# Kernel optimization log

Measured on AMD Instinct MI355X. Metric: run time of the kernel, lower is better.

Reference implementation:

```python
import jax, jax.numpy as jnp
import numpy as np

E = 524288
B = 16
NODE_IN = 128
EDGE_IN = 64
GLOBAL_IN = 64
HIDDEN = 256
EDGE_OUT = 64
CAT_IN = EDGE_IN + 2 * NODE_IN + GLOBAL_IN  # 384


def setup_inputs() -> dict:
    key = jax.random.key(0)
    ks = jax.random.split(key, 9)
    src = jax.random.normal(ks[0], (E, NODE_IN), dtype=jnp.float32)
    dest = jax.random.normal(ks[1], (E, NODE_IN), dtype=jnp.float32)
    edge_attr = jax.random.normal(ks[2], (E, EDGE_IN), dtype=jnp.float32)
    u = jax.random.normal(ks[3], (B, GLOBAL_IN), dtype=jnp.float32)
    batch = jnp.sort(jax.random.randint(ks[4], (E,), 0, B, dtype=jnp.int64))
    # MLP params (torch Linear default init scale ~1/sqrt(fan_in))
    W1 = jax.random.normal(ks[5], (CAT_IN, HIDDEN), dtype=jnp.float32) / np.sqrt(CAT_IN)
    b1 = jax.random.normal(ks[6], (HIDDEN,), dtype=jnp.float32) / np.sqrt(CAT_IN)
    W2 = jax.random.normal(ks[7], (HIDDEN, EDGE_OUT), dtype=jnp.float32) / np.sqrt(HIDDEN)
    b2 = jax.random.normal(ks[8], (EDGE_OUT,), dtype=jnp.float32) / np.sqrt(HIDDEN)
    return {"src": src, "dest": dest, "edge_attr": edge_attr, "u": u,
            "batch": batch, "W1": W1, "b1": b1, "W2": W2, "b2": b2}


def reference(src, dest, edge_attr, u, batch, W1, b1, W2, b2):
    # gather global features per edge, concat, 2-layer MLP with ReLU
    x = jnp.concatenate([src, dest, edge_attr, u[batch]], axis=1)  # [E, 384]
    h = jax.nn.relu(x @ W1 + b1)                                   # [E, hidden]
    return h @ W2 + b2                                             # [E, edge_out]
```

## Files before the change

kernel.cpp:

```cpp
#include <hip/hip_runtime.h>

typedef __bf16 bf16_t;
typedef bf16_t bf16x8 __attribute__((ext_vector_type(8)));
typedef bf16_t bf16x4 __attribute__((ext_vector_type(4)));
typedef float f32x4 __attribute__((ext_vector_type(4)));
typedef unsigned short u16;
typedef unsigned int u32;

#define E_TOT 524288
#define MT 64
#define NBLK (E_TOT / MT)

__device__ __forceinline__ u16 f2bf(float f) {
  u32 u = __builtin_bit_cast(u32, f);
  u += 0x7FFFu + ((u >> 16) & 1u);
  return (u16)(u >> 16);
}

__device__ __forceinline__ bf16x8 pack8(f32x4 a, f32x4 b) {
  bf16x8 p;
  p[0] = (bf16_t)a[0]; p[1] = (bf16_t)a[1]; p[2] = (bf16_t)a[2]; p[3] = (bf16_t)a[3];
  p[4] = (bf16_t)b[0]; p[5] = (bf16_t)b[1]; p[6] = (bf16_t)b[2]; p[7] = (bf16_t)b[3];
  return p;
}

__global__ void prep_w1f(const float* __restrict__ W1, u16* __restrict__ W1F) {
  int t = blockIdx.x * 256 + threadIdx.x;
  if (t < 98304) {
    int e  = t & 7;
    int l  = (t >> 3) & 63;
    int nf = (t >> 9) & 3;
    int wc = (t >> 11) & 3;
    int kb = t >> 13;
    int n = wc * 64 + nf * 16 + (l & 15);
    int k = kb * 32 + ((l >> 4) << 3) + e;
    W1F[t] = f2bf(W1[k * 256 + n]);
  }
}

__global__ void prep_w2f(const float* __restrict__ W2, u16* __restrict__ W2F) {
  int t = blockIdx.x * 256 + threadIdx.x;
  if (t < 16384) {
    int e   = t & 7;
    int l   = (t >> 3) & 63;
    int n2f = (t >> 9) & 3;
    int ks  = t >> 11;
    int n2 = n2f * 16 + (l & 15);
    int k  = ks * 32 + ((l >> 4) << 3) + e;
    W2F[t] = f2bf(W2[k * 64 + n2]);
  }
}

__global__ void __launch_bounds__(256) edge_fused(
    const float* __restrict__ src, const float* __restrict__ dst,
    const float* __restrict__ ea, const float* __restrict__ u,
    const int* __restrict__ batch, const u16* __restrict__ W1F,
    const float* __restrict__ b1, const u16* __restrict__ W2F,
    const float* __restrict__ b2, float* __restrict__ out)
{
  __shared__ __align__(16) u16 smem[16384];
  u16* As = smem;
  u16* Hs = smem;

  const int t    = threadIdx.x;
  const int wid  = t >> 6;
  const int lane = t & 63;
  const int lr   = lane & 15;
  const int lg   = lane >> 4;
  const int e0   = blockIdx.x * MT;
  const int r    = t >> 2;
  const int jc   = t & 3;
  const int bidx = batch[e0 + r];
  const int u0   = 2 * jc;

  auto loadA = [&](int c, f32x4* ra) {
    const float* p;
    if (c < 2)       p = src + (size_t)(e0 + r) * 128 + c * 64 + jc * 16;
    else if (c < 4)  p = dst + (size_t)(e0 + r) * 128 + (c - 2) * 64 + jc * 16;
    else if (c == 4) p = ea + (size_t)(e0 + r) * 64 + jc * 16;
    else             p = u + (size_t)bidx * 64 + jc * 16;
    ra[0] = *(const f32x4*)p;
    ra[1] = *(const f32x4*)(p + 4);
    ra[2] = *(const f32x4*)(p + 8);
    ra[3] = *(const f32x4*)(p + 12);
  };
  auto loadW1 = [&](int c, bf16x8* wf) {
    #pragma unroll
    for (int ks = 0; ks < 2; ++ks) {
      const u16* p = W1F + ((size_t)((2 * c + ks) * 4 + wid) * 4) * 512 + lane * 8;
      wf[ks * 4 + 0] = *(const bf16x8*)(p);
      wf[ks * 4 + 1] = *(const bf16x8*)(p + 512);
      wf[ks * 4 + 2] = *(const bf16x8*)(p + 1024);
      wf[ks * 4 + 3] = *(const bf16x8*)(p + 1536);
    }
  };

  f32x4 ra[4];
  bf16x8 wf[8];
  loadA(0, ra);
  loadW1(0, wf);

  f32x4 acc[4][4];
  #pragma unroll
  for (int i = 0; i < 4; ++i)
    #pragma unroll
    for (int j = 0; j < 4; ++j)
      acc[i][j] = (f32x4){0.f, 0.f, 0.f, 0.f};

  #pragma unroll
  for (int kb = 0; kb < 6; ++kb) {
    u16* Ab = As + (kb & 1) * 4096;

    {
      bf16x8 lo = pack8(ra[0], ra[1]);
      bf16x8 hi = pack8(ra[2], ra[3]);
      *(bf16x8*)&Ab[(r * 8 + (u0 ^ (r & 7))) * 8]       = lo;
      *(bf16x8*)&Ab[(r * 8 + ((u0 + 1) ^ (r & 7))) * 8] = hi;
    }
    if (kb < 5) loadA(kb + 1, ra);

    asm volatile("s_waitcnt lgkmcnt(0)" ::: "memory");
    __builtin_amdgcn_s_barrier();
    __builtin_amdgcn_sched_barrier(0);

    __builtin_amdgcn_s_setprio(1);
    #pragma unroll
    for (int ks = 0; ks < 2; ++ks) {
      bf16x8 af[4];
      #pragma unroll
      for (int mf = 0; mf < 4; ++mf) {
        int row = mf * 16 + lr;
        af[mf] = *(const bf16x8*)&Ab[(row * 8 + ((ks * 4 + lg) ^ (row & 7))) * 8];
      }
      #pragma unroll
      for (int nf = 0; nf < 4; ++nf)
        #pragma unroll
        for (int mf = 0; mf < 4; ++mf)
          acc[nf][mf] = __builtin_amdgcn_mfma_f32_16x16x32_bf16(wf[ks * 4 + nf], af[mf], acc[nf][mf], 0, 0, 0);
    }
    __builtin_amdgcn_s_setprio(0);

    if (kb < 5) loadW1(kb + 1, wf);
  }
  __syncthreads();

  #pragma unroll
  for (int nf = 0; nf < 4; ++nf) {
    f32x4 b1v = *(const f32x4*)(b1 + wid * 64 + nf * 16 + lg * 4);
    #pragma unroll
    for (int mf = 0; mf < 4; ++mf) {
      int row = mf * 16 + lr;
      bf16x4 hb;
      #pragma unroll
      for (int rr = 0; rr < 4; ++rr)
        hb[rr] = (bf16_t)fmaxf(acc[nf][mf][rr] + b1v[rr], 0.f);
      int uu = (wid * 4 + nf) * 4 + lg;
      int up = uu ^ ((lr & 3) << 2);
      *(bf16x4*)&Hs[row * 256 + up * 4] = hb;
    }
  }
  __syncthreads();

  const int row2 = wid * 16 + lr;
  f32x4 d2[4];
  #pragma unroll
  for (int i = 0; i < 4; ++i) d2[i] = (f32x4){0.f, 0.f, 0.f, 0.f};
  #pragma unroll
  for (int ks = 0; ks < 8; ++ks) {
    int uu = ks * 8 + lg * 2;
    int up = uu ^ ((lr & 3) << 2);
    bf16x8 a2 = *(const bf16x8*)&Hs[row2 * 256 + up * 4];
    const u16* q = W2F + (size_t)ks * 2048 + lane * 8;
    #pragma unroll
    for (int n2f = 0; n2f < 4; ++n2f)
      d2[n2f] = __builtin_amdgcn_mfma_f32_16x16x32_bf16(
          *(const bf16x8*)(q + n2f * 512), a2, d2[n2f], 0, 0, 0);
  }

  #pragma unroll
  for (int n2f = 0; n2f < 4; ++n2f) {
    f32x4 b2v = *(const f32x4*)(b2 + n2f * 16 + lg * 4);
    f32x4 ov = d2[n2f] + b2v;
    *(f32x4*)&out[(size_t)(e0 + row2) * 64 + n2f * 16 + lg * 4] = ov;
  }
}

extern "C" void kernel_launch(void* const* d_in, const int* in_sizes, int n_in,
                              void* d_out, int out_size, void* d_ws, size_t ws_size,
                              hipStream_t stream) {
  const float* src  = (const float*)d_in[0];
  const float* dst  = (const float*)d_in[1];
  const float* ea   = (const float*)d_in[2];
  const float* u    = (const float*)d_in[3];
  const int* batch  = (const int*)d_in[4];
  const float* W1   = (const float*)d_in[5];
  const float* b1   = (const float*)d_in[6];
  const float* W2   = (const float*)d_in[7];
  const float* b2   = (const float*)d_in[8];
  float* out = (float*)d_out;

  u16* W1F = (u16*)d_ws;
  u16* W2F = W1F + 98304;

  prep_w1f<<<384, 256, 0, stream>>>(W1, W1F);
  prep_w2f<<<64, 256, 0, stream>>>(W2, W2F);
  edge_fused<<<NBLK, 256, 0, stream>>>(src, dst, ea, u, batch, W1F, b1, W2F, b2, out);
}
```

Measured before the change: 243.6 us.

## Make edge kernel persistent over several tiles with cross-tile prefetch

Each block now processes 8 consecutive 64-edge tiles in a loop instead of one, cutting the grid by 8x. Input loads are double-buffered two chunks ahead, and the first chunks and W1 fragments of the next tile are prefetched during the tail of the current tile, so global loads overlap the MFMA and epilogue phases. The cost is more registers for the extra prefetch buffer and far fewer blocks, which may leave CUs underfilled or idle at the tail and lowers occupancy.

```diff
diff --git a/kernel.cpp b/kernel.cpp
--- a/kernel.cpp
+++ b/kernel.cpp
@@ -9,7 +9,8 @@
 
 #define E_TOT 524288
 #define MT 64
-#define NBLK (E_TOT / MT)
+#define TPB 8
+#define NBLK (E_TOT / (MT * TPB))
 
 __device__ __forceinline__ u16 f2bf(float f) {
   u32 u = __builtin_bit_cast(u32, f);
@@ -67,18 +68,18 @@
   const int lane = t & 63;
   const int lr   = lane & 15;
   const int lg   = lane >> 4;
-  const int e0   = blockIdx.x * MT;
   const int r    = t >> 2;
   const int jc   = t & 3;
-  const int bidx = batch[e0 + r];
   const int u0   = 2 * jc;
-
-  auto loadA = [&](int c, f32x4* ra) {
+  const int eb0  = blockIdx.x * (MT * TPB);
+
+  auto loadA = [&](int c, int ebase, f32x4* ra) {
+    size_t er = (size_t)(ebase + r);
     const float* p;
-    if (c < 2)       p = src + (size_t)(e0 + r) * 128 + c * 64 + jc * 16;
-    else if (c < 4)  p = dst + (size_t)(e0 + r) * 128 + (c - 2) * 64 + jc * 16;
-    else if (c == 4) p = ea + (size_t)(e0 + r) * 64 + jc * 16;
-    else             p = u + (size_t)bidx * 64 + jc * 16;
+    if (c < 2)       p = src + er * 128 + c * 64 + jc * 16;
+    else if (c < 4)  p = dst + er * 128 + (c - 2) * 64 + jc * 16;
+    else if (c == 4) p = ea + er * 64 + jc * 16;
+    else             p = u + (size_t)batch[er] * 64 + jc * 16;
     ra[0] = *(const f32x4*)p;
     ra[1] = *(const f32x4*)(p + 4);
     ra[2] = *(const f32x4*)(p + 8);
@@ -95,93 +96,113 @@
     }
   };
 
-  f32x4 ra[4];
+  f32x4 ra[4], rb[4];
   bf16x8 wf[8];
-  loadA(0, ra);
+  loadA(0, eb0, ra);
+  loadA(1, eb0, rb);
   loadW1(0, wf);
 
-  f32x4 acc[4][4];
-  #pragma unroll
-  for (int i = 0; i < 4; ++i)
-    #pragma unroll
-    for (int j = 0; j < 4; ++j)
-      acc[i][j] = (f32x4){0.f, 0.f, 0.f, 0.f};
-
-  #pragma unroll
-  for (int kb = 0; kb < 6; ++kb) {
-    u16* Ab = As + (kb & 1) * 4096;
-
-    {
-      bf16x8 lo = pack8(ra[0], ra[1]);
-      bf16x8 hi = pack8(ra[2], ra[3]);
-      *(bf16x8*)&Ab[(r * 8 + (u0 ^ (r & 7))) * 8]       = lo;
-      *(bf16x8*)&Ab[(r * 8 + ((u0 + 1) ^ (r & 7))) * 8] = hi;
-    }
-    if (kb < 5) loadA(kb + 1, ra);
+  for (int tile = 0; tile < TPB; ++tile) {
+    const int eb = eb0 + tile * MT;
+
+    f32x4 acc[4][4];
+    #pragma unroll
+    for (int i = 0; i < 4; ++i)
+      #pragma unroll
+      for (int j = 0; j < 4; ++j)
+        acc[i][j] = (f32x4){0.f, 0.f, 0.f, 0.f};
+
+    #pragma unroll
+    for (int c = 0; c < 6; ++c) {
+      f32x4* cur = (c & 1) ? rb : ra;
+      u16* Ab = As + (c & 1) * 4096;
+
+      {
+        bf16x8 lo = pack8(cur[0], cur[1]);
+        bf16x8 hi = pack8(cur[2], cur[3]);
+        *(bf16x8*)&Ab[(r * 8 + (u0 ^ (r & 7))) * 8]       = lo;
+        *(bf16x8*)&Ab[(r * 8 + ((u0 + 1) ^ (r & 7))) * 8] = hi;
+      }
+      if (c < 4)            loadA(c + 2, eb, cur);
+      else if (tile < TPB - 1) {
+        if (c == 4) loadA(0, eb + MT, cur);
+        else        loadA(1, eb + MT, cur);
+      }
+
+      asm volatile("s_waitcnt lgkmcnt(0)" ::: "memory");
+      __builtin_amdgcn_s_barrier();
+      __builtin_amdgcn_sched_barrier(0);
+
+      __builtin_amdgcn_s_setprio(1);
+      #pragma unroll
+      for (int ks = 0; ks < 2; ++ks) {
+        bf16x8 af[4];
+        #pragma unroll
+        for (int mf = 0; mf < 4; ++mf) {
+          int row = mf * 16 + lr;
+          af[mf] = *(const bf16x8*)&Ab[(row * 8 + ((ks * 4 + lg) ^ (row & 7))) * 8];
+        }
+        #pragma unroll
+        for (int nf = 0; nf < 4; ++nf)
+          #pragma unroll
+          for (int mf = 0; mf < 4; ++mf)
+            acc[nf][mf] = __builtin_amdgcn_mfma_f32_16x16x32_bf16(wf[ks * 4 + nf], af[mf], acc[nf][mf], 0, 0, 0);
+      }
+      __builtin_amdgcn_s_setprio(0);
+
+      if (c < 5)                loadW1(c + 1, wf);
+      else if (tile < TPB - 1)  loadW1(0, wf);
+    }
 
     asm volatile("s_waitcnt lgkmcnt(0)" ::: "memory");
     __builtin_amdgcn_s_barrier();
     __builtin_amdgcn_sched_barrier(0);
 
-    __builtin_amdgcn_s_setprio(1);
-    #pragma unroll
-    for (int ks = 0; ks < 2; ++ks) {
-      bf16x8 af[4];
+    #pragma unroll
+    for (int nf = 0; nf < 4; ++nf) {
+      f32x4 b1v = *(const f32x4*)(b1 + wid * 64 + nf * 16 + lg * 4);
       #pragma unroll
       for (int mf = 0; mf < 4; ++mf) {
+        bf16x4 hb;
+        #pragma unroll
+        for (int rr = 0; rr < 4; ++rr)
+          hb[rr] = (bf16_t)fmaxf(acc[nf][mf][rr] + b1v[rr], 0.f);
         int row = mf * 16 + lr;
-        af[mf] = *(const bf16x8*)&Ab[(row * 8 + ((ks * 4 + lg) ^ (row & 7))) * 8];
-      }
-      #pragma unroll
-      for (int nf = 0; nf < 4; ++nf)
-        #pragma unroll
-        for (int mf = 0; mf < 4; ++mf)
-          acc[nf][mf] = __builtin_amdgcn_mfma_f32_16x16x32_bf16(wf[ks * 4 + nf], af[mf], acc[nf][mf], 0, 0, 0);
-    }
-    __builtin_amdgcn_s_setprio(0);
-
-    if (kb < 5) loadW1(kb + 1, wf);
-  }
-  __syncthreads();
-
-  #pragma unroll
-  for (int nf = 0; nf < 4; ++nf) {
-    f32x4 b1v = *(const f32x4*)(b1 + wid * 64 + nf * 16 + lg * 4);
-    #pragma unroll
-    for (int mf = 0; mf < 4; ++mf) {
-      int row = mf * 16 + lr;
-      bf16x4 hb;
-      #pragma unroll
-      for (int rr = 0; rr < 4; ++rr)
-        hb[rr] = (bf16_t)fmaxf(acc[nf][mf][rr] + b1v[rr], 0.f);
-      int uu = (wid * 4 + nf) * 4 + lg;
+        int uu = (wid * 4 + nf) * 4 + lg;
+        int up = uu ^ ((lr & 3) << 2);
+        *(bf16x4*)&Hs[row * 256 + up * 4] = hb;
+      }
+    }
+    asm volatile("s_waitcnt lgkmcnt(0)" ::: "memory");
+    __builtin_amdgcn_s_barrier();
+    __builtin_amdgcn_sched_barrier(0);
+
+    const int row2 = wid * 16 + lr;
+    f32x4 d2[4];
+    #pragma unroll
+    for (int i = 0; i < 4; ++i) d2[i] = (f32x4){0.f, 0.f, 0.f, 0.f};
+    #pragma unroll
+    for (int ks = 0; ks < 8; ++ks) {
+      int uu = ks * 8 + lg * 2;
       int up = uu ^ ((lr & 3) << 2);
-      *(bf16x4*)&Hs[row * 256 + up * 4] = hb;
-    }
-  }
-  __syncthreads();
-
-  const int row2 = wid * 16 + lr;
-  f32x4 d2[4];
-  #pragma unroll
-  for (int i = 0; i < 4; ++i) d2[i] = (f32x4){0.f, 0.f, 0.f, 0.f};
-  #pragma unroll
-  for (int ks = 0; ks < 8; ++ks) {
-    int uu = ks * 8 + lg * 2;
-    int up = uu ^ ((lr & 3) << 2);
-    bf16x8 a2 = *(const bf16x8*)&Hs[row2 * 256 + up * 4];
-    const u16* q = W2F + (size_t)ks * 2048 + lane * 8;
-    #pragma unroll
-    for (int n2f = 0; n2f < 4; ++n2f)
-      d2[n2f] = __builtin_amdgcn_mfma_f32_16x16x32_bf16(
-          *(const bf16x8*)(q + n2f * 512), a2, d2[n2f], 0, 0, 0);
-  }
-
-  #pragma unroll
-  for (int n2f = 0; n2f < 4; ++n2f) {
-    f32x4 b2v = *(const f32x4*)(b2 + n2f * 16 + lg * 4);
-    f32x4 ov = d2[n2f] + b2v;
-    *(f32x4*)&out[(size_t)(e0 + row2) * 64 + n2f * 16 + lg * 4] = ov;
+      bf16x8 a2 = *(const bf16x8*)&Hs[row2 * 256 + up * 4];
+      const u16* q = W2F + (size_t)ks * 2048 + lane * 8;
+      #pragma unroll
+      for (int n2f = 0; n2f < 4; ++n2f)
+        d2[n2f] = __builtin_amdgcn_mfma_f32_16x16x32_bf16(
+            *(const bf16x8*)(q + n2f * 512), a2, d2[n2f], 0, 0, 0);
+    }
+
+    #pragma unroll
+    for (int n2f = 0; n2f < 4; ++n2f) {
+      f32x4 b2v = *(const f32x4*)(b2 + n2f * 16 + lg * 4);
+      f32x4 ov = d2[n2f] + b2v;
+      *(f32x4*)&out[(size_t)(eb + row2) * 64 + n2f * 16 + lg * 4] = ov;
+    }
+
+    asm volatile("s_waitcnt lgkmcnt(0)" ::: "memory");
+    __builtin_amdgcn_s_barrier();
+    __builtin_amdgcn_sched_barrier(0);
   }
 }
 
```

After: 405.9 us. +66.6%, slower.

## Enlarge edge tile to 128 rows with 8 waves and LDS-staged W1 pipeline

Applied to the files above, without the earlier changes.

Doubles the block tile to 128 edges with 512 threads in a 2x4 wave grid. W1 is now staged into LDS with global_load_lds, double-buffered and swizzled, rather than each wave loading its fragments from global memory into registers. A three-deep register prefetch of A chunks is added, the N dimension is split into two halves separated by barriers, and block indices are remapped so consecutive blocks are spread across the edge range. The aim is better W1 reuse across more rows and more overlap of loads with MFMA, at the cost of 96KB of LDS per block, which lowers occupancy, plus more barriers.

```diff
diff --git a/kernel.cpp b/kernel.cpp
--- a/kernel.cpp
+++ b/kernel.cpp
@@ -8,8 +8,8 @@
 typedef unsigned int u32;
 
 #define E_TOT 524288
-#define MT 64
-#define NBLK (E_TOT / MT)
+#define BM 128
+#define NBLK (E_TOT / BM)
 
 __device__ __forceinline__ u16 f2bf(float f) {
   u32 u = __builtin_bit_cast(u32, f);
@@ -24,17 +24,22 @@
   return p;
 }
 
-__global__ void prep_w1f(const float* __restrict__ W1, u16* __restrict__ W1F) {
+__device__ __forceinline__ void gload_lds16(const void* g, void* l) {
+  __builtin_amdgcn_global_load_lds(
+      (const __attribute__((address_space(1))) u32*)g,
+      (__attribute__((address_space(3))) u32*)l, 16, 0, 0);
+}
+
+__global__ void prep_w1c(const float* __restrict__ W1, u16* __restrict__ W1c) {
   int t = blockIdx.x * 256 + threadIdx.x;
   if (t < 98304) {
-    int e  = t & 7;
-    int l  = (t >> 3) & 63;
-    int nf = (t >> 9) & 3;
-    int wc = (t >> 11) & 3;
-    int kb = t >> 13;
-    int n = wc * 64 + nf * 16 + (l & 15);
-    int k = kb * 32 + ((l >> 4) << 3) + e;
-    W1F[t] = f2bf(W1[k * 256 + n]);
+    int e = t & 7;
+    int U = t >> 3;
+    int kb = U >> 11, rem = U & 2047;
+    int n = rem >> 3, jswz = rem & 7;
+    int j = jswz ^ (n & 7);
+    int k = kb * 64 + j * 8 + e;
+    W1c[t] = f2bf(W1[k * 256 + n]);
   }
 }
 
@@ -51,15 +56,14 @@
   }
 }
 
-__global__ void __launch_bounds__(256) edge_fused(
+__global__ void __launch_bounds__(512) edge_fused(
     const float* __restrict__ src, const float* __restrict__ dst,
     const float* __restrict__ ea, const float* __restrict__ u,
-    const int* __restrict__ batch, const u16* __restrict__ W1F,
+    const int* __restrict__ batch, const u16* __restrict__ W1c,
     const float* __restrict__ b1, const u16* __restrict__ W2F,
     const float* __restrict__ b2, float* __restrict__ out)
 {
-  __shared__ __align__(16) u16 smem[16384];
-  u16* As = smem;
+  __shared__ __align__(16) u16 smem[49152];
   u16* Hs = smem;
 
   const int t    = threadIdx.x;
@@ -67,38 +71,51 @@
   const int lane = t & 63;
   const int lr   = lane & 15;
   const int lg   = lane >> 4;
-  const int e0   = blockIdx.x * MT;
+  const int wr   = wid >> 2;
+  const int wc   = wid & 3;
+  const int bid  = blockIdx.x;
+  const int e0   = ((bid & 7) * 512 + (bid >> 3)) * BM;
   const int r    = t >> 2;
   const int jc   = t & 3;
+  const int j0   = 2 * jc;
   const int bidx = batch[e0 + r];
-  const int u0   = 2 * jc;
-
-  auto loadA = [&](int c, f32x4* ra) {
+
+  auto loadA = [&](int c, f32x4* s) {
     const float* p;
     if (c < 2)       p = src + (size_t)(e0 + r) * 128 + c * 64 + jc * 16;
     else if (c < 4)  p = dst + (size_t)(e0 + r) * 128 + (c - 2) * 64 + jc * 16;
     else if (c == 4) p = ea + (size_t)(e0 + r) * 64 + jc * 16;
     else             p = u + (size_t)bidx * 64 + jc * 16;
-    ra[0] = *(const f32x4*)p;
-    ra[1] = *(const f32x4*)(p + 4);
-    ra[2] = *(const f32x4*)(p + 8);
-    ra[3] = *(const f32x4*)(p + 12);
+    s[0] = *(const f32x4*)p;
+    s[1] = *(const f32x4*)(p + 4);
+    s[2] = *(const f32x4*)(p + 8);
+    s[3] = *(const f32x4*)(p + 12);
   };
-  auto loadW1 = [&](int c, bf16x8* wf) {
-    #pragma unroll
-    for (int ks = 0; ks < 2; ++ks) {
-      const u16* p = W1F + ((size_t)((2 * c + ks) * 4 + wid) * 4) * 512 + lane * 8;
-      wf[ks * 4 + 0] = *(const bf16x8*)(p);
-      wf[ks * 4 + 1] = *(const bf16x8*)(p + 512);
-      wf[ks * 4 + 2] = *(const bf16x8*)(p + 1024);
-      wf[ks * 4 + 3] = *(const bf16x8*)(p + 1536);
+  auto issueW = [&](int c, u16* Wn) {
+    #pragma unroll
+    for (int g = 0; g < 4; ++g) {
+      int ub = wid * 256 + g * 64;
+      gload_lds16(W1c + ((size_t)c * 2048 + ub + lane) * 8, Wn + ub * 8);
     }
   };
-
-  f32x4 ra[4];
-  bf16x8 wf[8];
-  loadA(0, ra);
-  loadW1(0, wf);
+  auto packWrite = [&](f32x4* s, u16* An) {
+    bf16x8 lo = pack8(s[0], s[1]);
+    bf16x8 hi = pack8(s[2], s[3]);
+    *(bf16x8*)&An[(r * 8 + (j0 ^ (r & 7))) * 8]       = lo;
+    *(bf16x8*)&An[(r * 8 + ((j0 + 1) ^ (r & 7))) * 8] = hi;
+  };
+
+  f32x4 aset[3][4];
+  loadA(0, aset[0]);
+  loadA(1, aset[1]);
+  issueW(0, smem + 16384);
+  loadA(2, aset[2]);
+  asm volatile("s_waitcnt vmcnt(12)" ::: "memory");
+  packWrite(aset[0], smem);
+  asm volatile("s_waitcnt vmcnt(4)" ::: "memory");
+  asm volatile("s_waitcnt lgkmcnt(0)" ::: "memory");
+  __builtin_amdgcn_sched_barrier(0);
+  __builtin_amdgcn_s_barrier();
 
   f32x4 acc[4][4];
   #pragma unroll
@@ -109,57 +126,89 @@
 
   #pragma unroll
   for (int kb = 0; kb < 6; ++kb) {
-    u16* Ab = As + (kb & 1) * 4096;
-
-    {
-      bf16x8 lo = pack8(ra[0], ra[1]);
-      bf16x8 hi = pack8(ra[2], ra[3]);
-      *(bf16x8*)&Ab[(r * 8 + (u0 ^ (r & 7))) * 8]       = lo;
-      *(bf16x8*)&Ab[(r * 8 + ((u0 + 1) ^ (r & 7))) * 8] = hi;
-    }
-    if (kb < 5) loadA(kb + 1, ra);
+    u16* Ab = smem + ((kb & 1) << 13);
+    u16* An = smem + (((kb + 1) & 1) << 13);
+    u16* Wb = smem + 16384 + ((kb & 1) << 14);
+    u16* Wn = smem + 16384 + (((kb + 1) & 1) << 14);
+
+    bf16x8 af[2][4];
+    #pragma unroll
+    for (int ks = 0; ks < 2; ++ks)
+      #pragma unroll
+      for (int mf = 0; mf < 4; ++mf) {
+        int row = wr * 64 + mf * 16 + lr;
+        af[ks][mf] = *(const bf16x8*)&Ab[(row * 8 + ((ks * 4 + lg) ^ (row & 7))) * 8];
+      }
+    bf16x8 wf0[2][2];
+    #pragma unroll
+    for (int ks = 0; ks < 2; ++ks)
+      #pragma unroll
+      for (int nfi = 0; nfi < 2; ++nfi) {
+        int n = wc * 64 + nfi * 16 + lr;
+        wf0[ks][nfi] = *(const bf16x8*)&Wb[(n * 8 + ((ks * 4 + lg) ^ (n & 7))) * 8];
+      }
+    if (kb < 5) issueW(kb + 1, Wn);
 
     asm volatile("s_waitcnt lgkmcnt(0)" ::: "memory");
-    __builtin_amdgcn_s_barrier();
     __builtin_amdgcn_sched_barrier(0);
-
+    __builtin_amdgcn_s_barrier();
     __builtin_amdgcn_s_setprio(1);
     #pragma unroll
-    for (int ks = 0; ks < 2; ++ks) {
-      bf16x8 af[4];
-      #pragma unroll
-      for (int mf = 0; mf < 4; ++mf) {
-        int row = mf * 16 + lr;
-        af[mf] = *(const bf16x8*)&Ab[(row * 8 + ((ks * 4 + lg) ^ (row & 7))) * 8];
-      }
-      #pragma unroll
-      for (int nf = 0; nf < 4; ++nf)
+    for (int nfi = 0; nfi < 2; ++nfi)
+      #pragma unroll
+      for (int ks = 0; ks < 2; ++ks)
         #pragma unroll
         for (int mf = 0; mf < 4; ++mf)
-          acc[nf][mf] = __builtin_amdgcn_mfma_f32_16x16x32_bf16(wf[ks * 4 + nf], af[mf], acc[nf][mf], 0, 0, 0);
-    }
+          acc[nfi][mf] = __builtin_amdgcn_mfma_f32_16x16x32_bf16(wf0[ks][nfi], af[ks][mf], acc[nfi][mf], 0, 0, 0);
     __builtin_amdgcn_s_setprio(0);
-
-    if (kb < 5) loadW1(kb + 1, wf);
-  }
-  __syncthreads();
+    __builtin_amdgcn_s_barrier();
+
+    bf16x8 wf1[2][2];
+    #pragma unroll
+    for (int ks = 0; ks < 2; ++ks)
+      #pragma unroll
+      for (int nfi = 0; nfi < 2; ++nfi) {
+        int n = wc * 64 + (2 + nfi) * 16 + lr;
+        wf1[ks][nfi] = *(const bf16x8*)&Wb[(n * 8 + ((ks * 4 + lg) ^ (n & 7))) * 8];
+      }
+    if (kb < 5) packWrite(aset[(kb + 1) % 3], An);
+    if (kb < 3) loadA(kb + 3, aset[(kb + 3) % 3]);
+
+    if (kb < 3)      asm volatile("s_waitcnt vmcnt(4)" ::: "memory");
+    else if (kb < 5) asm volatile("s_waitcnt vmcnt(0)" ::: "memory");
+    asm volatile("s_waitcnt lgkmcnt(0)" ::: "memory");
+    __builtin_amdgcn_sched_barrier(0);
+    __builtin_amdgcn_s_barrier();
+    __builtin_amdgcn_s_setprio(1);
+    #pragma unroll
+    for (int nfi = 0; nfi < 2; ++nfi)
+      #pragma unroll
+      for (int ks = 0; ks < 2; ++ks)
+        #pragma unroll
+        for (int mf = 0; mf < 4; ++mf)
+          acc[2 + nfi][mf] = __builtin_amdgcn_mfma_f32_16x16x32_bf16(wf1[ks][nfi], af[ks][mf], acc[2 + nfi][mf], 0, 0, 0);
+    __builtin_amdgcn_s_setprio(0);
+    __builtin_amdgcn_s_barrier();
+  }
 
   #pragma unroll
   for (int nf = 0; nf < 4; ++nf) {
-    f32x4 b1v = *(const f32x4*)(b1 + wid * 64 + nf * 16 + lg * 4);
+    f32x4 b1v = *(const f32x4*)(b1 + wc * 64 + nf * 16 + lg * 4);
     #pragma unroll
     for (int mf = 0; mf < 4; ++mf) {
-      int row = mf * 16 + lr;
       bf16x4 hb;
       #pragma unroll
       for (int rr = 0; rr < 4; ++rr)
         hb[rr] = (bf16_t)fmaxf(acc[nf][mf][rr] + b1v[rr], 0.f);
-      int uu = (wid * 4 + nf) * 4 + lg;
+      int row = wr * 64 + mf * 16 + lr;
+      int uu = (wc * 4 + nf) * 4 + lg;
       int up = uu ^ ((lr & 3) << 2);
       *(bf16x4*)&Hs[row * 256 + up * 4] = hb;
     }
   }
-  __syncthreads();
+  asm volatile("s_waitcnt lgkmcnt(0)" ::: "memory");
+  __builtin_amdgcn_sched_barrier(0);
+  __builtin_amdgcn_s_barrier();
 
   const int row2 = wid * 16 + lr;
   f32x4 d2[4];
@@ -199,10 +248,10 @@
   const float* b2   = (const float*)d_in[8];
   float* out = (float*)d_out;
 
-  u16* W1F = (u16*)d_ws;
-  u16* W2F = W1F + 98304;
-
-  prep_w1f<<<384, 256, 0, stream>>>(W1, W1F);
+  u16* W1c = (u16*)d_ws;
+  u16* W2F = W1c + 98304;
+
+  prep_w1c<<<384, 256, 0, stream>>>(W1, W1c);
   prep_w2f<<<64, 256, 0, stream>>>(W2, W2F);
-  edge_fused<<<NBLK, 256, 0, stream>>>(src, dst, ea, u, batch, W1F, b1, W2F, b2, out);
-}
+  edge_fused<<<NBLK, 512, 0, stream>>>(src, dst, ea, u, batch, W1c, b1, W2F, b2, out);
+}
```

Result: slower. 286.0 us (+17.4%).
